# Kernel tuning notes

Hardware: AMD Instinct MI355X
Metric: run time of the kernel (lower is better)

The kernel has to match this reference:

```python
import jax, jax.numpy as jnp
import numpy as np

D_MODEL = 1024
D_KV = 64
N_HEADS = 16
INNER = N_HEADS * D_KV
EPS = 1e-6


def setup_inputs() -> dict:
    key = jax.random.key(0)
    ks = jax.random.split(key, 8)
    B, SQ, SKV = 2, 2048, 4096
    hidden_states = jax.random.normal(ks[0], (B, SQ, D_MODEL), dtype=jnp.float32)
    key_value_states = jax.random.normal(ks[1], (B, SKV, D_MODEL), dtype=jnp.float32)
    attention_mask = jnp.zeros((B, 1, 1, SKV), dtype=jnp.float32)
    # nn.Linear(in, out, bias=False): y = x @ W.T; store W as [in, out] here
    s = 0.02
    Wq = jax.random.normal(ks[2], (D_MODEL, INNER), dtype=jnp.float32) * s
    Wk = jax.random.normal(ks[3], (D_MODEL, INNER), dtype=jnp.float32) * s
    Wv = jax.random.normal(ks[4], (D_MODEL, INNER), dtype=jnp.float32) * s
    Wo = jax.random.normal(ks[5], (INNER, D_MODEL), dtype=jnp.float32) * s
    ln_weight = jnp.ones((D_MODEL,), dtype=jnp.float32)
    return {
        "hidden_states": hidden_states,
        "key_value_states": key_value_states,
        "attention_mask": attention_mask,
        "ln_weight": ln_weight,
        "Wq": Wq,
        "Wk": Wk,
        "Wv": Wv,
        "Wo": Wo,
    }


def _t5_rmsnorm(x, w, eps=EPS):
    # no mean subtraction, variance in fp32
    var = jnp.mean(jnp.square(x.astype(jnp.float32)), axis=-1, keepdims=True)
    return w * (x * jax.lax.rsqrt(var + eps)).astype(x.dtype)


def reference(hidden_states, key_value_states, attention_mask, ln_weight, Wq, Wk, Wv, Wo):
    B, SQ, _ = hidden_states.shape
    SKV = key_value_states.shape[1]
    normed = _t5_rmsnorm(hidden_states, ln_weight)

    # projections -> [B, H, S, Dk]
    q = (normed @ Wq).reshape(B, SQ, N_HEADS, D_KV).transpose(0, 2, 1, 3)
    k = (key_value_states @ Wk).reshape(B, SKV, N_HEADS, D_KV).transpose(0, 2, 1, 3)
    v = (key_value_states @ Wv).reshape(B, SKV, N_HEADS, D_KV).transpose(0, 2, 1, 3)

    # T5: NO 1/sqrt(d) scaling
    scores = jnp.einsum("bhqd,bhkd->bhqk", q, k) + attention_mask
    attn = jax.nn.softmax(scores.astype(jnp.float32), axis=-1).astype(scores.dtype)
    ctx = jnp.einsum("bhqk,bhkd->bhqd", attn, v)
    ctx = ctx.transpose(0, 2, 1, 3).reshape(B, SQ, INNER)
    attn_out = ctx @ Wo
    return hidden_states + attn_out
```

## Files before the change

kernel.cpp:

```cpp
#include <hip/hip_runtime.h>

typedef unsigned short u16;
typedef unsigned int u32;
typedef __attribute__((ext_vector_type(4))) float f32x4;
typedef __attribute__((ext_vector_type(8))) short short8;

#define BB   2
#define SQL  2048
#define SKVL 4096
#define DM   1024
#define NH   16
#define DK   64
#define L2E  1.44269504f

#if __has_builtin(__builtin_amdgcn_exp2f)
#define EXP2(x) __builtin_amdgcn_exp2f(x)
#else
#define EXP2(x) exp2f(x)
#endif

__device__ __forceinline__ u16 f2bf(float f) {
  union { float f; unsigned u; } v; v.f = f;
  unsigned r = v.u + 0x7fff + ((v.u >> 16) & 1);
  return (u16)(r >> 16);
}

__device__ __forceinline__ void gload16(const void* g, void* lds) {
  __builtin_amdgcn_global_load_lds(
      (const __attribute__((address_space(1))) unsigned int*)g,
      (__attribute__((address_space(3))) unsigned int*)lds, 16, 0, 0);
}

#define MFMA(a, b, c) __builtin_amdgcn_mfma_f32_16x16x32_bf16(a, b, c, 0, 0, 0)

__global__ void rmsnorm_kernel(const float* __restrict__ x, const float* __restrict__ w,
                               u16* __restrict__ out) {
  int row = blockIdx.x;
  int t = threadIdx.x;
  float4 v = ((const float4*)(x + (size_t)row * DM))[t];
  float ss = v.x * v.x + v.y * v.y + v.z * v.z + v.w * v.w;
#pragma unroll
  for (int m = 32; m >= 1; m >>= 1) ss += __shfl_xor(ss, m, 64);
  __shared__ float red[4];
  int lane = t & 63, wv = t >> 6;
  if (lane == 0) red[wv] = ss;
  __syncthreads();
  float total = red[0] + red[1] + red[2] + red[3];
  float scale = rsqrtf(total * (1.0f / DM) + 1e-6f);
  float4 g = ((const float4*)w)[t];
  ushort4 o;
  o.x = f2bf(v.x * scale * g.x);
  o.y = f2bf(v.y * scale * g.y);
  o.z = f2bf(v.z * scale * g.z);
  o.w = f2bf(v.w * scale * g.w);
  ((ushort4*)(out + (size_t)row * DM))[t] = o;
}

__global__ void cvt_kernel(const float* __restrict__ in, u16* __restrict__ out) {
  int i = blockIdx.x * 256 + threadIdx.x;
  float4 v = ((const float4*)in)[i];
  ushort4 o;
  o.x = f2bf(v.x); o.y = f2bf(v.y); o.z = f2bf(v.z); o.w = f2bf(v.w);
  ((ushort4*)out)[i] = o;
}

__global__ void tcvt4_kernel(const float* __restrict__ W0, const float* __restrict__ W1,
                             const float* __restrict__ W2, const float* __restrict__ W3,
                             u16* __restrict__ O0, u16* __restrict__ O1,
                             u16* __restrict__ O2, u16* __restrict__ O3) {
  const float* W; u16* Wt;
  switch (blockIdx.z) {
    case 0: W = W0; Wt = O0; break;
    case 1: W = W1; Wt = O1; break;
    case 2: W = W2; Wt = O2; break;
    default: W = W3; Wt = O3; break;
  }
  __shared__ float tile[32][33];
  int tx = threadIdx.x & 31, ty = threadIdx.x >> 5;
  int k0 = blockIdx.y * 32, n0 = blockIdx.x * 32;
#pragma unroll
  for (int i = 0; i < 4; i++)
    tile[ty + i * 8][tx] = W[(size_t)(k0 + ty + i * 8) * DM + n0 + tx];
  __syncthreads();
#pragma unroll
  for (int i = 0; i < 4; i++)
    Wt[(size_t)(n0 + ty + i * 8) * DM + k0 + tx] = f2bf(tile[tx][ty + i * 8]);
}

template <int MODE>
__global__ void gemm_kernel(const u16* __restrict__ A, const u16* __restrict__ Bt,
                            void* __restrict__ C, const float* __restrict__ aux,
                            int N, float scale) {
  const int K = 1024;
  __shared__ __align__(16) u16 Al[128 * 32];
  __shared__ __align__(16) u16 Bl[128 * 32];
  int tid = threadIdx.x, lane = tid & 63, w = tid >> 6;
  int l15 = lane & 15, quad = lane >> 4;
  int wy = w >> 1, wx = w & 1;
  int tm = blockIdx.x * 128, tn = blockIdx.y * 128;
  f32x4 acc[4][4] = {};

  for (int k0 = 0; k0 < K; k0 += 32) {
    __syncthreads();
#pragma unroll
    for (int r = 0; r < 2; r++) {
      int mg = w * 2 + r;
      gload16(A + (size_t)(tm + mg * 16 + l15) * K + k0 + quad * 8, &Al[mg * 512]);
      gload16(Bt + (size_t)(tn + mg * 16 + l15) * K + k0 + quad * 8, &Bl[mg * 512]);
    }
    __syncthreads();
    short8 af[4], bfr[4];
#pragma unroll
    for (int i = 0; i < 4; i++) {
      af[i] = *(const short8*)&Al[((wy * 4 + i) * 64 + lane) * 8];
      bfr[i] = *(const short8*)&Bl[((wx * 4 + i) * 64 + lane) * 8];
    }
#pragma unroll
    for (int mt = 0; mt < 4; mt++)
#pragma unroll
      for (int nt = 0; nt < 4; nt++)
        acc[mt][nt] = MFMA(af[mt], bfr[nt], acc[mt][nt]);
  }

#pragma unroll
  for (int mt = 0; mt < 4; mt++) {
    int m0 = tm + wy * 64 + mt * 16 + quad * 4;
#pragma unroll
    for (int nt = 0; nt < 4; nt++) {
      int n = tn + wx * 64 + nt * 16 + l15;
      if (MODE == 0) {
#pragma unroll
        for (int r = 0; r < 4; r++)
          ((u16*)C)[(size_t)(m0 + r) * N + n] = f2bf(acc[mt][nt][r] * scale);
      } else {
#pragma unroll
        for (int r = 0; r < 4; r++) {
          size_t idx = (size_t)(m0 + r) * N + n;
          ((float*)C)[idx] = aux[idx] + acc[mt][nt][r];
        }
      }
    }
  }
}

__global__ void kvgemm_kernel(const u16* __restrict__ kvb, const u16* __restrict__ Wkt,
                              const u16* __restrict__ Wvt, u16* __restrict__ Kbf,
                              u16* __restrict__ Vtb, const float* __restrict__ mask) {
  const int K = 1024;
  __shared__ __align__(16) u16 Al[128 * 32];
  __shared__ __align__(16) u16 Bl[128 * 32];
  int tid = threadIdx.x, lane = tid & 63, w = tid >> 6;
  int l15 = lane & 15, quad = lane >> 4;
  int wy = w >> 1, wx = w & 1;

  int bid = blockIdx.x;
  bool vmode = bid >= 512;
  const u16 *A, *Bt;
  int tm, tn;
  if (!vmode) { A = kvb; Bt = Wkt; tm = (bid & 63) * 128; tn = (bid >> 6) * 128; }
  else { int vid = bid - 512; A = Wvt; Bt = kvb; tm = (vid & 7) * 128; tn = (vid >> 3) * 128; }

  f32x4 acc[4][4] = {};
  for (int k0 = 0; k0 < K; k0 += 32) {
    __syncthreads();
#pragma unroll
    for (int r = 0; r < 2; r++) {
      int mg = w * 2 + r;
      gload16(A + (size_t)(tm + mg * 16 + l15) * K + k0 + quad * 8, &Al[mg * 512]);
      gload16(Bt + (size_t)(tn + mg * 16 + l15) * K + k0 + quad * 8, &Bl[mg * 512]);
    }
    __syncthreads();
    short8 af[4], bfr[4];
#pragma unroll
    for (int i = 0; i < 4; i++) {
      af[i] = *(const short8*)&Al[((wy * 4 + i) * 64 + lane) * 8];
      bfr[i] = *(const short8*)&Bl[((wx * 4 + i) * 64 + lane) * 8];
    }
#pragma unroll
    for (int mt = 0; mt < 4; mt++)
#pragma unroll
      for (int nt = 0; nt < 4; nt++)
        acc[mt][nt] = MFMA(af[mt], bfr[nt], acc[mt][nt]);
  }

#pragma unroll
  for (int mt = 0; mt < 4; mt++) {
    int m0 = tm + wy * 64 + mt * 16 + quad * 4;
#pragma unroll
    for (int nt = 0; nt < 4; nt++) {
      int n = tn + wx * 64 + nt * 16 + l15;
      if (!vmode) {
#pragma unroll
        for (int r = 0; r < 4; r++)
          Kbf[(size_t)(m0 + r) * 1024 + n] = f2bf(acc[mt][nt][r]);
      } else {
        float pm = EXP2(mask[n] * L2E);
        int b = n >> 12, skv = n & 4095;
#pragma unroll
        for (int r = 0; r < 4; r++)
          Vtb[((size_t)(b * 1024 + m0 + r) << 12) + skv] = f2bf(acc[mt][nt][r] * pm);
      }
    }
  }
}

__global__ __launch_bounds__(256, 2) void flash_kernel(
    const u16* __restrict__ Qp, const u16* __restrict__ Kp, const u16* __restrict__ Vtp,
    const float* __restrict__ mask, u16* __restrict__ ctx) {
  __shared__ __align__(16) char smem[73728];
  u16* Kl2 = (u16*)smem;
  u16* Vl2 = (u16*)(smem + 16384);
  char* pl_base = smem + 32768;
  u16* pml = (u16*)(smem + 65536);
  float* Ox = (float*)smem;
  float* Ll = (float*)(smem + 32768);

  int tid = threadIdx.x, lane = tid & 63, w = tid >> 6;
  int l15 = lane & 15, quad = lane >> 4;
  int grp = w >> 1, wg = w & 1;
  int qb = blockIdx.x, bh = blockIdx.y;
  int b = bh >> 4, h = bh & 15;
  int q0 = qb * 128 + wg * 64;

  {
    int i0 = tid * 16;
#pragma unroll
    for (int g = 0; g < 4; g++) {
      float4 mv = *(const float4*)(mask + (size_t)b * SKVL + i0 + g * 4);
      ushort4 o;
      o.x = f2bf(EXP2(mv.x * L2E)); o.y = f2bf(EXP2(mv.y * L2E));
      o.z = f2bf(EXP2(mv.z * L2E)); o.w = f2bf(EXP2(mv.w * L2E));
      *(ushort4*)&pml[i0 + g * 4] = o;
    }
  }

  short8 qf[4][2];
#pragma unroll
  for (int mt = 0; mt < 4; mt++)
#pragma unroll
    for (int kf = 0; kf < 2; kf++)
      qf[mt][kf] = *(const short8*)(Qp + (size_t)(b * SQL + q0 + mt * 16 + l15) * DM +
                                    h * DK + kf * 32 + quad * 8);

  f32x4 of[4][4] = {};
  f32x4 la[4] = {};
  char* plw = pl_base + w * 8192;
  const int pbase = (quad >> 1) * 256 + (quad & 1) * 8 + l15 * 16;
  u16* Klg = Kl2 + grp * 4096;
  u16* Vlg = Vl2 + grp * 4096;

  for (int it = 0; it < 32; ++it) {
    int kv0 = it * 128 + grp * 64;
    __syncthreads();
#pragma unroll
    for (int r = 0; r < 4; r++) {
      int u = wg * 4 + r;
      int kt = u >> 1, kf = u & 1;
      gload16(Kp + (size_t)(b * SKVL + kv0 + kt * 16 + l15) * DM + h * DK + kf * 32 + quad * 8,
              &Klg[u * 512]);
      gload16(Vtp + (size_t)((b * NH + h) * DK + kt * 16 + l15) * SKVL + kv0 + kf * 32 + quad * 8,
              &Vlg[u * 512]);
    }
    __syncthreads();

#pragma unroll
    for (int kt = 0; kt < 4; kt++) {
      short8 k0 = *(const short8*)&Klg[((kt * 2 + 0) * 64 + lane) * 8];
      short8 k1 = *(const short8*)&Klg[((kt * 2 + 1) * 64 + lane) * 8];
#pragma unroll
      for (int mt = 0; mt < 4; mt++) {
        f32x4 st = {0.f, 0.f, 0.f, 0.f};
        st = MFMA(k0, qf[mt][0], st);
        st = MFMA(k1, qf[mt][1], st);
        union { float f; u32 u; } c0, c1, c2, c3;
        c0.f = EXP2(st[0]); c1.f = EXP2(st[1]);
        c2.f = EXP2(st[2]); c3.f = EXP2(st[3]);
        uint2 pk;
        pk.x = ((c0.u + 0x8000u) >> 16) | ((c1.u + 0x8000u) & 0xffff0000u);
        pk.y = ((c2.u + 0x8000u) >> 16) | ((c3.u + 0x8000u) & 0xffff0000u);
        *(uint2*)(plw + mt * 2048 + kt * 512 + pbase) = pk;
      }
    }
    asm volatile("s_waitcnt lgkmcnt(0)" ::: "memory");

#pragma unroll
    for (int kf = 0; kf < 2; kf++) {
      short8 pmf = *(const short8*)&pml[kv0 + kf * 32 + quad * 8];
      short8 pa[4];
#pragma unroll
      for (int mt = 0; mt < 4; mt++)
        pa[mt] = *(const short8*)(plw + ((mt * 2 + kf) * 4 + quad) * 256 + l15 * 16);
#pragma unroll
      for (int mt = 0; mt < 4; mt++) la[mt] = MFMA(pa[mt], pmf, la[mt]);
#pragma unroll
      for (int nt = 0; nt < 4; nt++) {
        short8 vf = *(const short8*)&Vlg[((nt * 2 + kf) * 64 + lane) * 8];
#pragma unroll
        for (int mt = 0; mt < 4; mt++)
          of[mt][nt] = MFMA(pa[mt], vf, of[mt][nt]);
      }
    }
  }

  __syncthreads();
  if (grp == 1) {
#pragma unroll
    for (int mt = 0; mt < 4; mt++) {
#pragma unroll
      for (int nt = 0; nt < 4; nt++)
#pragma unroll
        for (int r = 0; r < 4; r++)
          Ox[(wg * 64 + mt * 16 + quad * 4 + r) * 64 + nt * 16 + l15] = of[mt][nt][r];
      if (l15 == 0)
#pragma unroll
        for (int r = 0; r < 4; r++) Ll[wg * 64 + mt * 16 + quad * 4 + r] = la[mt][r];
    }
  }
  __syncthreads();
  if (grp == 0) {
#pragma unroll
    for (int mt = 0; mt < 4; mt++)
#pragma unroll
      for (int r = 0; r < 4; r++) {
        int ql = wg * 64 + mt * 16 + quad * 4 + r;
        float inv = 1.0f / (la[mt][r] + Ll[ql]);
        int q = qb * 128 + ql;
#pragma unroll
        for (int nt = 0; nt < 4; nt++) {
          float ov = of[mt][nt][r] + Ox[ql * 64 + nt * 16 + l15];
          ctx[(size_t)(b * SQL + q) * DM + h * DK + nt * 16 + l15] = f2bf(ov * inv);
        }
      }
  }
}

extern "C" void kernel_launch(void* const* d_in, const int* in_sizes, int n_in,
                              void* d_out, int out_size, void* d_ws, size_t ws_size,
                              hipStream_t stream) {
  const float* hidden = (const float*)d_in[0];
  const float* kvs    = (const float*)d_in[1];
  const float* mask   = (const float*)d_in[2];
  const float* lnw    = (const float*)d_in[3];
  const float* Wq     = (const float*)d_in[4];
  const float* Wk     = (const float*)d_in[5];
  const float* Wv     = (const float*)d_in[6];
  const float* Wo     = (const float*)d_in[7];
  char* ws = (char*)d_ws;

  u16* normed = (u16*)(ws + 0);
  u16* kvb    = (u16*)(ws + 8388608);
  u16* Wqt    = (u16*)(ws + 25165824);
  u16* Wkt    = (u16*)(ws + 27262976);
  u16* Wvt    = (u16*)(ws + 29360128);
  u16* Wot    = (u16*)(ws + 31457280);
  u16* Qb     = (u16*)(ws + 33554432);
  u16* Kbf    = (u16*)(ws + 41943040);
  u16* Vtb    = (u16*)(ws + 58720256);
  u16* ctxb   = (u16*)(ws + 75497472);

  rmsnorm_kernel<<<BB * SQL, 256, 0, stream>>>(hidden, lnw, normed);
  cvt_kernel<<<(BB * SKVL * DM) / 1024, 256, 0, stream>>>(kvs, kvb);
  tcvt4_kernel<<<dim3(32, 32, 4), 256, 0, stream>>>(Wq, Wk, Wv, Wo, Wqt, Wkt, Wvt, Wot);

  gemm_kernel<0><<<dim3(32, 8), 256, 0, stream>>>(normed, Wqt, Qb, nullptr, 1024, L2E);
  kvgemm_kernel<<<1024, 256, 0, stream>>>(kvb, Wkt, Wvt, Kbf, Vtb, mask);

  flash_kernel<<<dim3(SQL / 128, BB * NH), 256, 0, stream>>>(Qb, Kbf, Vtb, mask, ctxb);

  gemm_kernel<2><<<dim3(32, 8), 256, 0, stream>>>(ctxb, Wot, d_out, hidden, 1024, 1.0f);
}
```

Baseline: 350.9 us.

## Fuse prep kernels, merge projections, register-resident P with double-buffered flash loads

Merges the rmsnorm, input conversion and weight transpose kernels into one launch, and the Q/K/V projection GEMMs into one launch, so fewer kernels run. In the flash kernel, the probabilities are fed to 16x16x16 MFMAs straight from registers instead of passing through LDS. V is pre-swizzled into a fragment-ready layout and K/V tiles are double-buffered so the next tile loads while the current one computes. The row sum is accumulated in scalar adds with the mask added inside the exponent, replacing the extra MFMA for row sums. This uses more LDS and more VALU adds, and relies on a new V layout.

```diff
diff --git a/kernel.cpp b/kernel.cpp
--- a/kernel.cpp
+++ b/kernel.cpp
@@ -4,6 +4,7 @@
 typedef unsigned int u32;
 typedef __attribute__((ext_vector_type(4))) float f32x4;
 typedef __attribute__((ext_vector_type(8))) short short8;
+typedef __attribute__((ext_vector_type(4))) short short4v;
 
 #define BB   2
 #define SQL  2048
@@ -19,78 +20,294 @@
 #define EXP2(x) exp2f(x)
 #endif
 
+#define MFMA32(a, b, c) __builtin_amdgcn_mfma_f32_16x16x32_bf16(a, b, c, 0, 0, 0)
+#define MFMA16(a, b, c) __builtin_amdgcn_mfma_f32_16x16x16bf16_1k(a, b, c, 0, 0, 0)
+
 __device__ __forceinline__ u16 f2bf(float f) {
   union { float f; unsigned u; } v; v.f = f;
   unsigned r = v.u + 0x7fff + ((v.u >> 16) & 1);
   return (u16)(r >> 16);
 }
 
+__device__ __forceinline__ short4v pack4(float p0, float p1, float p2, float p3) {
+  union { float f; u32 u; } a, b, c, d;
+  a.f = p0; b.f = p1; c.f = p2; d.f = p3;
+  union { uint2 v; short4v s; } r;
+  r.v.x = ((a.u + 0x8000u) >> 16) | ((b.u + 0x8000u) & 0xffff0000u);
+  r.v.y = ((c.u + 0x8000u) >> 16) | ((d.u + 0x8000u) & 0xffff0000u);
+  return r.s;
+}
+
 __device__ __forceinline__ void gload16(const void* g, void* lds) {
   __builtin_amdgcn_global_load_lds(
       (const __attribute__((address_space(1))) unsigned int*)g,
       (__attribute__((address_space(3))) unsigned int*)lds, 16, 0, 0);
 }
 
-#define MFMA(a, b, c) __builtin_amdgcn_mfma_f32_16x16x32_bf16(a, b, c, 0, 0, 0)
-
-__global__ void rmsnorm_kernel(const float* __restrict__ x, const float* __restrict__ w,
-                               u16* __restrict__ out) {
-  int row = blockIdx.x;
-  int t = threadIdx.x;
-  float4 v = ((const float4*)(x + (size_t)row * DM))[t];
-  float ss = v.x * v.x + v.y * v.y + v.z * v.z + v.w * v.w;
-#pragma unroll
-  for (int m = 32; m >= 1; m >>= 1) ss += __shfl_xor(ss, m, 64);
+__global__ void pre_kernel(const float* __restrict__ hidden, const float* __restrict__ lnw,
+                           const float* __restrict__ kvs,
+                           const float* __restrict__ Wq, const float* __restrict__ Wk,
+                           const float* __restrict__ Wv, const float* __restrict__ Wo,
+                           u16* __restrict__ normed, u16* __restrict__ kvb,
+                           u16* __restrict__ Wqt, u16* __restrict__ Wkt,
+                           u16* __restrict__ Wvt, u16* __restrict__ Wot) {
   __shared__ float red[4];
-  int lane = t & 63, wv = t >> 6;
-  if (lane == 0) red[wv] = ss;
+  __shared__ float tile[32][33];
+  int bid = blockIdx.x, t = threadIdx.x;
+  if (bid < 4096) {
+    int row = bid;
+    float4 v = ((const float4*)(hidden + (size_t)row * DM))[t];
+    float ss = v.x * v.x + v.y * v.y + v.z * v.z + v.w * v.w;
+#pragma unroll
+    for (int m = 32; m >= 1; m >>= 1) ss += __shfl_xor(ss, m, 64);
+    int lane = t & 63, wv = t >> 6;
+    if (lane == 0) red[wv] = ss;
+    __syncthreads();
+    float total = red[0] + red[1] + red[2] + red[3];
+    float scale = rsqrtf(total * (1.0f / DM) + 1e-6f);
+    float4 g = ((const float4*)lnw)[t];
+    ushort4 o;
+    o.x = f2bf(v.x * scale * g.x);
+    o.y = f2bf(v.y * scale * g.y);
+    o.z = f2bf(v.z * scale * g.z);
+    o.w = f2bf(v.w * scale * g.w);
+    ((ushort4*)(normed + (size_t)row * DM))[t] = o;
+  } else if (bid < 12288) {
+    int i = (bid - 4096) * 256 + t;
+    float4 v = ((const float4*)kvs)[i];
+    ushort4 o;
+    o.x = f2bf(v.x); o.y = f2bf(v.y); o.z = f2bf(v.z); o.w = f2bf(v.w);
+    ((ushort4*)kvb)[i] = o;
+  } else {
+    int g = bid - 12288;
+    int z = g >> 10;
+    const float* W = (z == 0) ? Wq : (z == 1) ? Wk : (z == 2) ? Wv : Wo;
+    u16* Wt = (z == 0) ? Wqt : (z == 1) ? Wkt : (z == 2) ? Wvt : Wot;
+    int xx = g & 31, yy = (g >> 5) & 31;
+    int tx = t & 31, ty = t >> 5;
+    int k0 = yy * 32, n0 = xx * 32;
+#pragma unroll
+    for (int i = 0; i < 4; i++)
+      tile[ty + i * 8][tx] = W[(size_t)(k0 + ty + i * 8) * DM + n0 + tx];
+    __syncthreads();
+#pragma unroll
+    for (int i = 0; i < 4; i++)
+      Wt[(size_t)(n0 + ty + i * 8) * DM + k0 + tx] = f2bf(tile[tx][ty + i * 8]);
+  }
+}
+
+__global__ void proj_kernel(const u16* __restrict__ normed, const u16* __restrict__ kvb,
+                            const u16* __restrict__ Wqt, const u16* __restrict__ Wkt,
+                            const u16* __restrict__ Wvt,
+                            u16* __restrict__ Qb, u16* __restrict__ Kbf,
+                            u16* __restrict__ Vtb) {
+  const int K = 1024;
+  __shared__ __align__(16) u16 Al[128 * 32];
+  __shared__ __align__(16) u16 Bl[128 * 32];
+  int tid = threadIdx.x, lane = tid & 63, w = tid >> 6;
+  int l15 = lane & 15, quad = lane >> 4;
+  int wy = w >> 1, wx = w & 1;
+
+  int bid = blockIdx.x;
+  int mode;
+  const u16 *A, *Bt;
+  int tm, tn;
+  if (bid < 256) { mode = 0; A = normed; Bt = Wqt; tm = (bid & 31) * 128; tn = (bid >> 5) * 128; }
+  else if (bid < 768) { mode = 1; A = kvb; Bt = Wkt; int kid = bid - 256; tm = (kid & 63) * 128; tn = (kid >> 6) * 128; }
+  else { mode = 2; A = Wvt; Bt = kvb; int vid = bid - 768; tm = (vid & 7) * 128; tn = (vid >> 3) * 128; }
+
+  f32x4 acc[4][4] = {};
+  for (int k0 = 0; k0 < K; k0 += 32) {
+    __syncthreads();
+#pragma unroll
+    for (int r = 0; r < 2; r++) {
+      int mg = w * 2 + r;
+      gload16(A + (size_t)(tm + mg * 16 + l15) * K + k0 + quad * 8, &Al[mg * 512]);
+      gload16(Bt + (size_t)(tn + mg * 16 + l15) * K + k0 + quad * 8, &Bl[mg * 512]);
+    }
+    __syncthreads();
+    short8 af[4], bfr[4];
+#pragma unroll
+    for (int i = 0; i < 4; i++) {
+      af[i] = *(const short8*)&Al[((wy * 4 + i) * 64 + lane) * 8];
+      bfr[i] = *(const short8*)&Bl[((wx * 4 + i) * 64 + lane) * 8];
+    }
+#pragma unroll
+    for (int mt = 0; mt < 4; mt++)
+#pragma unroll
+      for (int nt = 0; nt < 4; nt++)
+        acc[mt][nt] = MFMA32(af[mt], bfr[nt], acc[mt][nt]);
+  }
+
+#pragma unroll
+  for (int mt = 0; mt < 4; mt++) {
+    int m0 = tm + wy * 64 + mt * 16 + quad * 4;
+#pragma unroll
+    for (int nt = 0; nt < 4; nt++) {
+      int n = tn + wx * 64 + nt * 16 + l15;
+      if (mode == 0) {
+#pragma unroll
+        for (int r = 0; r < 4; r++)
+          Qb[(size_t)(m0 + r) * 1024 + n] = f2bf(acc[mt][nt][r] * L2E);
+      } else if (mode == 1) {
+#pragma unroll
+        for (int r = 0; r < 4; r++)
+          Kbf[(size_t)(m0 + r) * 1024 + n] = f2bf(acc[mt][nt][r]);
+      } else {
+        int b = n >> 12, skv = n & 4095;
+        int kvt = skv >> 6, kvl = skv & 63;
+        int p = kvl >> 5, kth = (kvl >> 4) & 1, qd = (kvl >> 2) & 3, elo = kvl & 3;
+        int e = kth * 4 + elo;
+        int h = m0 >> 6, d0 = m0 & 63;
+        size_t base = ((size_t)((b * NH + h) * 64 + kvt) << 12) + (size_t)(p * 4 + qd) * 512 + e;
+#pragma unroll
+        for (int r = 0; r < 4; r++)
+          Vtb[base + (size_t)(d0 + r) * 8] = f2bf(acc[mt][nt][r]);
+      }
+    }
+  }
+}
+
+__global__ __launch_bounds__(256, 2) void flash_kernel(
+    const u16* __restrict__ Qp, const u16* __restrict__ Kp, const u16* __restrict__ Vtb,
+    const float* __restrict__ mask, u16* __restrict__ ctx) {
+  __shared__ __align__(16) char smem[81920];
+  u16* Kbuf = (u16*)smem;
+  u16* Vbuf = (u16*)(smem + 32768);
+  float* mlog = (float*)(smem + 65536);
+  float* Ox = (float*)smem;
+  float* Ll = (float*)(smem + 32768);
+
+  int tid = threadIdx.x, lane = tid & 63, w = tid >> 6;
+  int l15 = lane & 15, quad = lane >> 4;
+  int grp = w >> 1, wg = w & 1;
+  int qb = blockIdx.x, bh = blockIdx.y;
+  int b = bh >> 4, h = bh & 15;
+  int q0 = qb * 128 + wg * 64;
+
+  {
+    const float* mrow = mask + (size_t)b * SKVL + tid * 16;
+#pragma unroll
+    for (int g = 0; g < 4; g++) {
+      float4 mv = *(const float4*)(mrow + g * 4);
+      float4 o; o.x = mv.x * L2E; o.y = mv.y * L2E; o.z = mv.z * L2E; o.w = mv.w * L2E;
+      *(float4*)&mlog[tid * 16 + g * 4] = o;
+    }
+  }
+
+  short8 qf[4][2];
+#pragma unroll
+  for (int mt = 0; mt < 4; mt++)
+#pragma unroll
+    for (int kf = 0; kf < 2; kf++)
+      qf[mt][kf] = *(const short8*)(Qp + (size_t)(b * SQL + q0 + mt * 16 + l15) * DM +
+                                    h * DK + kf * 32 + quad * 8);
+
+  f32x4 of[4][4] = {};
+  float ls[4] = {0.f, 0.f, 0.f, 0.f};
+
+  const size_t vblob = (size_t)(b * NH + h) * 64 * 4096;
+
+  auto stage = [&](int tileIdx, int buf) {
+    int kv0 = tileIdx * 64;
+    u16* Kd = Kbuf + (buf * 2 + grp) * 4096;
+    u16* Vd = Vbuf + (buf * 2 + grp) * 4096;
+#pragma unroll
+    for (int r = 0; r < 4; r++) {
+      int u = wg * 4 + r;
+      int kt = u >> 1, kf = u & 1;
+      gload16(Kp + (size_t)(b * SKVL + kv0 + kt * 16 + l15) * DM + h * DK + kf * 32 + quad * 8,
+              &Kd[u * 512]);
+      gload16(Vtb + vblob + (size_t)tileIdx * 4096 + u * 512 + lane * 8, &Vd[u * 512]);
+    }
+  };
+
+  stage(grp, 0);
+  for (int it = 0; it < 32; ++it) {
+    __syncthreads();
+    if (it + 1 < 32) stage((it + 1) * 2 + grp, (it + 1) & 1);
+    int tileIdx = it * 2 + grp;
+    int kv0 = tileIdx * 64;
+    const u16* Kg = Kbuf + ((it & 1) * 2 + grp) * 4096;
+    const u16* Vg = Vbuf + ((it & 1) * 2 + grp) * 4096;
+
+#pragma unroll
+    for (int ktp = 0; ktp < 2; ktp++) {
+      short4v pa[2][4];
+#pragma unroll
+      for (int kth = 0; kth < 2; kth++) {
+        int kt = ktp * 2 + kth;
+        short8 k0 = *(const short8*)&Kg[((kt * 2 + 0) * 64 + lane) * 8];
+        short8 k1 = *(const short8*)&Kg[((kt * 2 + 1) * 64 + lane) * 8];
+        f32x4 ml = *(const f32x4*)&mlog[kv0 + kt * 16 + quad * 4];
+#pragma unroll
+        for (int mt = 0; mt < 4; mt++) {
+          f32x4 st = {0.f, 0.f, 0.f, 0.f};
+          st = MFMA32(k0, qf[mt][0], st);
+          st = MFMA32(k1, qf[mt][1], st);
+          float p0 = EXP2(st[0] + ml[0]);
+          float p1 = EXP2(st[1] + ml[1]);
+          float p2 = EXP2(st[2] + ml[2]);
+          float p3 = EXP2(st[3] + ml[3]);
+          ls[mt] += (p0 + p1) + (p2 + p3);
+          pa[kth][mt] = pack4(p0, p1, p2, p3);
+        }
+      }
+#pragma unroll
+      for (int nt = 0; nt < 4; nt++) {
+        short8 vv = *(const short8*)&Vg[((ktp * 4 + quad) * 64 + nt * 16 + l15) * 8];
+        short4v vlo = {vv[0], vv[1], vv[2], vv[3]};
+        short4v vhi = {vv[4], vv[5], vv[6], vv[7]};
+#pragma unroll
+        for (int mt = 0; mt < 4; mt++) {
+          of[mt][nt] = MFMA16(pa[0][mt], vlo, of[mt][nt]);
+          of[mt][nt] = MFMA16(pa[1][mt], vhi, of[mt][nt]);
+        }
+      }
+    }
+  }
+
+#pragma unroll
+  for (int mt = 0; mt < 4; mt++) {
+    ls[mt] += __shfl_xor(ls[mt], 16, 64);
+    ls[mt] += __shfl_xor(ls[mt], 32, 64);
+  }
+
   __syncthreads();
-  float total = red[0] + red[1] + red[2] + red[3];
-  float scale = rsqrtf(total * (1.0f / DM) + 1e-6f);
-  float4 g = ((const float4*)w)[t];
-  ushort4 o;
-  o.x = f2bf(v.x * scale * g.x);
-  o.y = f2bf(v.y * scale * g.y);
-  o.z = f2bf(v.z * scale * g.z);
-  o.w = f2bf(v.w * scale * g.w);
-  ((ushort4*)(out + (size_t)row * DM))[t] = o;
-}
-
-__global__ void cvt_kernel(const float* __restrict__ in, u16* __restrict__ out) {
-  int i = blockIdx.x * 256 + threadIdx.x;
-  float4 v = ((const float4*)in)[i];
-  ushort4 o;
-  o.x = f2bf(v.x); o.y = f2bf(v.y); o.z = f2bf(v.z); o.w = f2bf(v.w);
-  ((ushort4*)out)[i] = o;
-}
-
-__global__ void tcvt4_kernel(const float* __restrict__ W0, const float* __restrict__ W1,
-                             const float* __restrict__ W2, const float* __restrict__ W3,
-                             u16* __restrict__ O0, u16* __restrict__ O1,
-                             u16* __restrict__ O2, u16* __restrict__ O3) {
-  const float* W; u16* Wt;
-  switch (blockIdx.z) {
-    case 0: W = W0; Wt = O0; break;
-    case 1: W = W1; Wt = O1; break;
-    case 2: W = W2; Wt = O2; break;
-    default: W = W3; Wt = O3; break;
-  }
-  __shared__ float tile[32][33];
-  int tx = threadIdx.x & 31, ty = threadIdx.x >> 5;
-  int k0 = blockIdx.y * 32, n0 = blockIdx.x * 32;
-#pragma unroll
-  for (int i = 0; i < 4; i++)
-    tile[ty + i * 8][tx] = W[(size_t)(k0 + ty + i * 8) * DM + n0 + tx];
+  if (grp == 1) {
+#pragma unroll
+    for (int mt = 0; mt < 4; mt++) {
+#pragma unroll
+      for (int nt = 0; nt < 4; nt++)
+#pragma unroll
+        for (int r = 0; r < 4; r++)
+          Ox[(wg * 64 + mt * 16 + quad * 4 + r) * 64 + nt * 16 + l15] = of[mt][nt][r];
+      if (quad == 0) Ll[wg * 64 + mt * 16 + l15] = ls[mt];
+    }
+  }
   __syncthreads();
-#pragma unroll
-  for (int i = 0; i < 4; i++)
-    Wt[(size_t)(n0 + ty + i * 8) * DM + k0 + tx] = f2bf(tile[tx][ty + i * 8]);
-}
-
-template <int MODE>
-__global__ void gemm_kernel(const u16* __restrict__ A, const u16* __restrict__ Bt,
-                            void* __restrict__ C, const float* __restrict__ aux,
-                            int N, float scale) {
+  if (grp == 0) {
+#pragma unroll
+    for (int mt = 0; mt < 4; mt++) {
+      float lt = ls[mt] + Ll[wg * 64 + mt * 16 + l15];
+#pragma unroll
+      for (int r = 0; r < 4; r++) {
+        float lqr = __shfl(lt, quad * 4 + r, 64);
+        float inv = 1.0f / lqr;
+        int ql = wg * 64 + mt * 16 + quad * 4 + r;
+        int q = qb * 128 + ql;
+#pragma unroll
+        for (int nt = 0; nt < 4; nt++) {
+          float ov = of[mt][nt][r] + Ox[ql * 64 + nt * 16 + l15];
+          ctx[(size_t)(b * SQL + q) * DM + h * DK + nt * 16 + l15] = f2bf(ov * inv);
+        }
+      }
+    }
+  }
+}
+
+__global__ void ogemm_kernel(const u16* __restrict__ A, const u16* __restrict__ Bt,
+                             float* __restrict__ C, const float* __restrict__ resid) {
   const int K = 1024;
   __shared__ __align__(16) u16 Al[128 * 32];
   __shared__ __align__(16) u16 Bl[128 * 32];
@@ -119,7 +336,7 @@
     for (int mt = 0; mt < 4; mt++)
 #pragma unroll
       for (int nt = 0; nt < 4; nt++)
-        acc[mt][nt] = MFMA(af[mt], bfr[nt], acc[mt][nt]);
+        acc[mt][nt] = MFMA32(af[mt], bfr[nt], acc[mt][nt]);
   }
 
 #pragma unroll
@@ -128,209 +345,12 @@
 #pragma unroll
     for (int nt = 0; nt < 4; nt++) {
       int n = tn + wx * 64 + nt * 16 + l15;
-      if (MODE == 0) {
-#pragma unroll
-        for (int r = 0; r < 4; r++)
-          ((u16*)C)[(size_t)(m0 + r) * N + n] = f2bf(acc[mt][nt][r] * scale);
-      } else {
-#pragma unroll
-        for (int r = 0; r < 4; r++) {
-          size_t idx = (size_t)(m0 + r) * N + n;
-          ((float*)C)[idx] = aux[idx] + acc[mt][nt][r];
-        }
-      }
-    }
-  }
-}
-
-__global__ void kvgemm_kernel(const u16* __restrict__ kvb, const u16* __restrict__ Wkt,
-                              const u16* __restrict__ Wvt, u16* __restrict__ Kbf,
-                              u16* __restrict__ Vtb, const float* __restrict__ mask) {
-  const int K = 1024;
-  __shared__ __align__(16) u16 Al[128 * 32];
-  __shared__ __align__(16) u16 Bl[128 * 32];
-  int tid = threadIdx.x, lane = tid & 63, w = tid >> 6;
-  int l15 = lane & 15, quad = lane >> 4;
-  int wy = w >> 1, wx = w & 1;
-
-  int bid = blockIdx.x;
-  bool vmode = bid >= 512;
-  const u16 *A, *Bt;
-  int tm, tn;
-  if (!vmode) { A = kvb; Bt = Wkt; tm = (bid & 63) * 128; tn = (bid >> 6) * 128; }
-  else { int vid = bid - 512; A = Wvt; Bt = kvb; tm = (vid & 7) * 128; tn = (vid >> 3) * 128; }
-
-  f32x4 acc[4][4] = {};
-  for (int k0 = 0; k0 < K; k0 += 32) {
-    __syncthreads();
-#pragma unroll
-    for (int r = 0; r < 2; r++) {
-      int mg = w * 2 + r;
-      gload16(A + (size_t)(tm + mg * 16 + l15) * K + k0 + quad * 8, &Al[mg * 512]);
-      gload16(Bt + (size_t)(tn + mg * 16 + l15) * K + k0 + quad * 8, &Bl[mg * 512]);
-    }
-    __syncthreads();
-    short8 af[4], bfr[4];
-#pragma unroll
-    for (int i = 0; i < 4; i++) {
-      af[i] = *(const short8*)&Al[((wy * 4 + i) * 64 + lane) * 8];
-      bfr[i] = *(const short8*)&Bl[((wx * 4 + i) * 64 + lane) * 8];
-    }
-#pragma unroll
-    for (int mt = 0; mt < 4; mt++)
-#pragma unroll
-      for (int nt = 0; nt < 4; nt++)
-        acc[mt][nt] = MFMA(af[mt], bfr[nt], acc[mt][nt]);
-  }
-
-#pragma unroll
-  for (int mt = 0; mt < 4; mt++) {
-    int m0 = tm + wy * 64 + mt * 16 + quad * 4;
-#pragma unroll
-    for (int nt = 0; nt < 4; nt++) {
-      int n = tn + wx * 64 + nt * 16 + l15;
-      if (!vmode) {
-#pragma unroll
-        for (int r = 0; r < 4; r++)
-          Kbf[(size_t)(m0 + r) * 1024 + n] = f2bf(acc[mt][nt][r]);
-      } else {
-        float pm = EXP2(mask[n] * L2E);
-        int b = n >> 12, skv = n & 4095;
-#pragma unroll
-        for (int r = 0; r < 4; r++)
-          Vtb[((size_t)(b * 1024 + m0 + r) << 12) + skv] = f2bf(acc[mt][nt][r] * pm);
-      }
-    }
-  }
-}
-
-__global__ __launch_bounds__(256, 2) void flash_kernel(
-    const u16* __restrict__ Qp, const u16* __restrict__ Kp, const u16* __restrict__ Vtp,
-    const float* __restrict__ mask, u16* __restrict__ ctx) {
-  __shared__ __align__(16) char smem[73728];
-  u16* Kl2 = (u16*)smem;
-  u16* Vl2 = (u16*)(smem + 16384);
-  char* pl_base = smem + 32768;
-  u16* pml = (u16*)(smem + 65536);
-  float* Ox = (float*)smem;
-  float* Ll = (float*)(smem + 32768);
-
-  int tid = threadIdx.x, lane = tid & 63, w = tid >> 6;
-  int l15 = lane & 15, quad = lane >> 4;
-  int grp = w >> 1, wg = w & 1;
-  int qb = blockIdx.x, bh = blockIdx.y;
-  int b = bh >> 4, h = bh & 15;
-  int q0 = qb * 128 + wg * 64;
-
-  {
-    int i0 = tid * 16;
-#pragma unroll
-    for (int g = 0; g < 4; g++) {
-      float4 mv = *(const float4*)(mask + (size_t)b * SKVL + i0 + g * 4);
-      ushort4 o;
-      o.x = f2bf(EXP2(mv.x * L2E)); o.y = f2bf(EXP2(mv.y * L2E));
-      o.z = f2bf(EXP2(mv.z * L2E)); o.w = f2bf(EXP2(mv.w * L2E));
-      *(ushort4*)&pml[i0 + g * 4] = o;
-    }
-  }
-
-  short8 qf[4][2];
-#pragma unroll
-  for (int mt = 0; mt < 4; mt++)
-#pragma unroll
-    for (int kf = 0; kf < 2; kf++)
-      qf[mt][kf] = *(const short8*)(Qp + (size_t)(b * SQL + q0 + mt * 16 + l15) * DM +
-                                    h * DK + kf * 32 + quad * 8);
-
-  f32x4 of[4][4] = {};
-  f32x4 la[4] = {};
-  char* plw = pl_base + w * 8192;
-  const int pbase = (quad >> 1) * 256 + (quad & 1) * 8 + l15 * 16;
-  u16* Klg = Kl2 + grp * 4096;
-  u16* Vlg = Vl2 + grp * 4096;
-
-  for (int it = 0; it < 32; ++it) {
-    int kv0 = it * 128 + grp * 64;
-    __syncthreads();
-#pragma unroll
-    for (int r = 0; r < 4; r++) {
-      int u = wg * 4 + r;
-      int kt = u >> 1, kf = u & 1;
-      gload16(Kp + (size_t)(b * SKVL + kv0 + kt * 16 + l15) * DM + h * DK + kf * 32 + quad * 8,
-              &Klg[u * 512]);
-      gload16(Vtp + (size_t)((b * NH + h) * DK + kt * 16 + l15) * SKVL + kv0 + kf * 32 + quad * 8,
-              &Vlg[u * 512]);
-    }
-    __syncthreads();
-
-#pragma unroll
-    for (int kt = 0; kt < 4; kt++) {
-      short8 k0 = *(const short8*)&Klg[((kt * 2 + 0) * 64 + lane) * 8];
-      short8 k1 = *(const short8*)&Klg[((kt * 2 + 1) * 64 + lane) * 8];
-#pragma unroll
-      for (int mt = 0; mt < 4; mt++) {
-        f32x4 st = {0.f, 0.f, 0.f, 0.f};
-        st = MFMA(k0, qf[mt][0], st);
-        st = MFMA(k1, qf[mt][1], st);
-        union { float f; u32 u; } c0, c1, c2, c3;
-        c0.f = EXP2(st[0]); c1.f = EXP2(st[1]);
-        c2.f = EXP2(st[2]); c3.f = EXP2(st[3]);
-        uint2 pk;
-        pk.x = ((c0.u + 0x8000u) >> 16) | ((c1.u + 0x8000u) & 0xffff0000u);
-        pk.y = ((c2.u + 0x8000u) >> 16) | ((c3.u + 0x8000u) & 0xffff0000u);
-        *(uint2*)(plw + mt * 2048 + kt * 512 + pbase) = pk;
-      }
-    }
-    asm volatile("s_waitcnt lgkmcnt(0)" ::: "memory");
-
-#pragma unroll
-    for (int kf = 0; kf < 2; kf++) {
-      short8 pmf = *(const short8*)&pml[kv0 + kf * 32 + quad * 8];
-      short8 pa[4];
-#pragma unroll
-      for (int mt = 0; mt < 4; mt++)
-        pa[mt] = *(const short8*)(plw + ((mt * 2 + kf) * 4 + quad) * 256 + l15 * 16);
-#pragma unroll
-      for (int mt = 0; mt < 4; mt++) la[mt] = MFMA(pa[mt], pmf, la[mt]);
-#pragma unroll
-      for (int nt = 0; nt < 4; nt++) {
-        short8 vf = *(const short8*)&Vlg[((nt * 2 + kf) * 64 + lane) * 8];
-#pragma unroll
-        for (int mt = 0; mt < 4; mt++)
-          of[mt][nt] = MFMA(pa[mt], vf, of[mt][nt]);
-      }
-    }
-  }
-
-  __syncthreads();
-  if (grp == 1) {
-#pragma unroll
-    for (int mt = 0; mt < 4; mt++) {
-#pragma unroll
-      for (int nt = 0; nt < 4; nt++)
-#pragma unroll
-        for (int r = 0; r < 4; r++)
-          Ox[(wg * 64 + mt * 16 + quad * 4 + r) * 64 + nt * 16 + l15] = of[mt][nt][r];
-      if (l15 == 0)
-#pragma unroll
-        for (int r = 0; r < 4; r++) Ll[wg * 64 + mt * 16 + quad * 4 + r] = la[mt][r];
-    }
-  }
-  __syncthreads();
-  if (grp == 0) {
-#pragma unroll
-    for (int mt = 0; mt < 4; mt++)
 #pragma unroll
       for (int r = 0; r < 4; r++) {
-        int ql = wg * 64 + mt * 16 + quad * 4 + r;
-        float inv = 1.0f / (la[mt][r] + Ll[ql]);
-        int q = qb * 128 + ql;
-#pragma unroll
-        for (int nt = 0; nt < 4; nt++) {
-          float ov = of[mt][nt][r] + Ox[ql * 64 + nt * 16 + l15];
-          ctx[(size_t)(b * SQL + q) * DM + h * DK + nt * 16 + l15] = f2bf(ov * inv);
-        }
-      }
+        size_t idx = (size_t)(m0 + r) * 1024 + n;
+        C[idx] = resid[idx] + acc[mt][nt][r];
+      }
+    }
   }
 }
 
@@ -358,14 +378,9 @@
   u16* Vtb    = (u16*)(ws + 58720256);
   u16* ctxb   = (u16*)(ws + 75497472);
 
-  rmsnorm_kernel<<<BB * SQL, 256, 0, stream>>>(hidden, lnw, normed);
-  cvt_kernel<<<(BB * SKVL * DM) / 1024, 256, 0, stream>>>(kvs, kvb);
-  tcvt4_kernel<<<dim3(32, 32, 4), 256, 0, stream>>>(Wq, Wk, Wv, Wo, Wqt, Wkt, Wvt, Wot);
-
-  gemm_kernel<0><<<dim3(32, 8), 256, 0, stream>>>(normed, Wqt, Qb, nullptr, 1024, L2E);
-  kvgemm_kernel<<<1024, 256, 0, stream>>>(kvb, Wkt, Wvt, Kbf, Vtb, mask);
-
+  pre_kernel<<<16384, 256, 0, stream>>>(hidden, lnw, kvs, Wq, Wk, Wv, Wo,
+                                        normed, kvb, Wqt, Wkt, Wvt, Wot);
+  proj_kernel<<<1280, 256, 0, stream>>>(normed, kvb, Wqt, Wkt, Wvt, Qb, Kbf, Vtb);
   flash_kernel<<<dim3(SQL / 128, BB * NH), 256, 0, stream>>>(Qb, Kbf, Vtb, mask, ctxb);
-
-  gemm_kernel<2><<<dim3(32, 8), 256, 0, stream>>>(ctxb, Wot, d_out, hidden, 1024, 1.0f);
-}
+  ogemm_kernel<<<dim3(32, 8), 256, 0, stream>>>(ctxb, Wot, (float*)d_out, hidden);
+}
```

After: 330.0 us. -6.0%, faster.
